# Kernel optimization log

Hardware: AMD Instinct MI355X
Metric: run time of the kernel (lower is better)

The kernel has to match this reference:

```python
import jax, jax.numpy as jnp
import numpy as np

B, S, D, H, HS, FF, L, V = 8, 512, 512, 8, 64, 2048, 6, 1024
EPS = 1e-5


def _layer_norm(x, g, b):
    m = jnp.mean(x, axis=-1, keepdims=True)
    v = jnp.var(x, axis=-1, keepdims=True)
    return (x - m) * jax.lax.rsqrt(v + EPS) * g + b


def _pos_encoding(seq_len, d, dtype):
    # Faithful to source: exponent uses 2*i/seq_len (x.shape[seq_dim]), not d_model.
    pos = jnp.arange(seq_len, dtype=dtype)[:, None]
    i = jnp.arange(d)
    pe = pos / (10000.0 ** (2.0 * i.astype(dtype) / seq_len))
    return jnp.where(i % 2 == 0, jnp.sin(pe), jnp.cos(pe))


def setup_inputs() -> dict:
    key = jax.random.key(0)
    ks = jax.random.split(key, 16)
    tok_ids = jax.random.randint(ks[0], (B, S), 0, V)
    tokens = jax.nn.one_hot(tok_ids, V, dtype=jnp.float32)
    std = 0.02
    return {
        "tokens": tokens,
        "token_embeddings": jax.random.normal(ks[1], (V, D), jnp.float32),
        "qkv_w": jax.random.normal(ks[2], (L, H, D, 3 * HS), jnp.float32) * std,
        "qkv_b": jnp.zeros((L, H, 3 * HS), jnp.float32),
        "out_w": jax.random.normal(ks[3], (L, D, D), jnp.float32) * std,
        "out_b": jnp.zeros((L, D), jnp.float32),
        "w1": jax.random.normal(ks[4], (L, D, FF), jnp.float32) * std,
        "b1": jnp.zeros((L, FF), jnp.float32),
        "w2": jax.random.normal(ks[5], (L, FF, D), jnp.float32) * std,
        "b2": jnp.zeros((L, D), jnp.float32),
        "ln1_g": jnp.ones((L, D), jnp.float32),
        "ln1_b": jnp.zeros((L, D), jnp.float32),
        "ln2_g": jnp.ones((L, D), jnp.float32),
        "ln2_b": jnp.zeros((L, D), jnp.float32),
    }


def _forward(tokens, token_embeddings, qkv_w, qkv_b, out_w, out_b,
             w1, b1, w2, b2, ln1_g, ln1_b, ln2_g, ln2_b):
    dt = tokens.dtype
    x = tokens @ (token_embeddings * (D ** 0.5))          # [B,S,D]
    x = x + _pos_encoding(S, D, dt)
    # Multiplicative causal mask (faithful to source: -1e6 strictly above diag, 0 elsewhere)
    mask = jnp.triu(jnp.full((S, S), -1e6, dt), k=1)
    scale = 1.0 / (HS ** 0.5)

    def block(x, p):
        (qw, qb, ow, ob, w1_, b1_, w2_, b2_, g1, be1, g2, be2) = p
        qkv = jnp.einsum('bsd,hdk->bhsk', x, qw) + qb[None, :, None, :]
        q, k, v = jnp.split(qkv, 3, axis=-1)              # each [B,H,S,HS]
        logits = jnp.einsum('bhsk,bhtk->bhst', q, k)      # [B,H,S,S]
        attn = jax.nn.softmax(logits * mask * scale, axis=-1)
        o = jnp.einsum('bhst,bhtk->bhsk', attn, v)
        o = o.transpose(0, 2, 1, 3).reshape(x.shape[0], S, D)  # concat heads
        o = o @ ow + ob
        x = _layer_norm(x + o, g1, be1)
        h = jax.nn.relu(x @ w1_ + b1_) @ w2_ + b2_
        x = _layer_norm(x + h, g2, be2)
        return x, None

    params = (qkv_w, qkv_b, out_w, out_b, w1, b1, w2, b2, ln1_g, ln1_b, ln2_g, ln2_b)
    x, _ = jax.lax.scan(block, x, params)
    return x @ token_embeddings.T                          # [B,S,V]


def reference(tokens, token_embeddings, qkv_w, qkv_b, out_w, out_b,
              w1, b1, w2, b2, ln1_g, ln1_b, ln2_g, ln2_b):
    return _forward(tokens, token_embeddings, qkv_w, qkv_b, out_w, out_b,
                    w1, b1, w2, b2, ln1_g, ln1_b, ln2_g, ln2_b)
```

## Files before the change

### kernel.cpp

```cpp
#include <hip/hip_runtime.h>
#include <math.h>

#define BB 8
#define SS 512
#define DD 512
#define HH 8
#define HSD 64
#define FFD 2048
#define LL 6
#define VV 1024
#define NROWS (BB*SS)
#define EPS 1e-5f

__global__ __launch_bounds__(256)
void embed_kernel(const float* __restrict__ tokens,
                  const float* __restrict__ emb,
                  float* __restrict__ x)
{
    const int n = blockIdx.x;
    const int s = n & (SS - 1);
    const int t = threadIdx.x;
    __shared__ int sidx;
    #pragma unroll
    for (int r = 0; r < 4; ++r) {
        int v = t + 256 * r;
        if (tokens[(long)n * VV + v] > 0.5f) sidx = v;
    }
    __syncthreads();
    const int idx = sidx;
    const float sq = 22.62741699796952f;
    #pragma unroll
    for (int r = 0; r < 2; ++r) {
        int d = t + 256 * r;
        float e = emb[(long)idx * DD + d] * sq;
        float expo  = (2.0f * (float)d) / 512.0f;
        float denom = powf(10000.0f, expo);
        float val   = (float)s / denom;
        float pe = ((d & 1) == 0) ? sinf(val) : cosf(val);
        x[(long)n * DD + d] = e + pe;
    }
}

__device__ __forceinline__ void gll16(const float* g, float* l)
{
    __builtin_amdgcn_global_load_lds(
        (const __attribute__((address_space(1))) void*)g,
        (__attribute__((address_space(3))) void*)l, 16, 0, 0);
}

template<int TNB, bool BT, bool QKVB, bool BIAS, bool RELU, bool RES>
__global__ __launch_bounds__(256)
void gemm_t(const float* __restrict__ A, const float* __restrict__ B,
            const float* __restrict__ bias, const float* __restrict__ res,
            float* __restrict__ C,
            int M, int N, int K, int lda, int ldb, int ldc)
{
    constexpr int NW   = TNB / 16;
    constexpr int BSTR = BT ? (TNB + 4) : TNB;
    constexpr int CPW  = TNB / 32;
    constexpr int CLOG = (TNB == 128) ? 7 : 6;
    const int t  = threadIdx.x;
    const int w  = t >> 6;
    const int ln = t & 63;
    const int bm = blockIdx.y * 128;
    const int bn = blockIdx.x * TNB;
    __shared__ float As[32][132];
    __shared__ __align__(16) float Bs[32][BSTR];
    const int tx = t & 15;
    const int ty = t >> 4;
    float acc[8][NW] = {};

    for (int k0 = 0; k0 < K; k0 += 32) {
        if (QKVB || !BT) {
            #pragma unroll
            for (int p = 0; p < CPW; ++p) {
                int ch = w * CPW + p;
                int fo = ch * 256 + ln * 4;
                int r  = fo >> CLOG;
                int c  = fo & (TNB - 1);
                const float* src;
                if (QKVB) {
                    int col = bn + c;
                    int hh = (int)((unsigned)col / 192u);
                    int j  = col - hh * 192;
                    src = B + (long)hh * (DD * 192) + (long)(k0 + r) * 192 + j;
                } else {
                    src = B + (long)(k0 + r) * ldb + bn + c;
                }
                gll16(src, &Bs[0][0] + ch * 256);
            }
        } else {
            #pragma unroll
            for (int p = 0; p < TNB / 32; ++p) {
                int q = t + 256 * p;
                int r = q >> 3, kc = (q & 7) * 4;
                float4 b4 = *(const float4*)(B + (long)(bn + r) * ldb + k0 + kc);
                Bs[kc + 0][r] = b4.x; Bs[kc + 1][r] = b4.y;
                Bs[kc + 2][r] = b4.z; Bs[kc + 3][r] = b4.w;
            }
        }
        #pragma unroll
        for (int p = 0; p < 4; ++p) {
            int q = t + 256 * p;
            int r = q >> 3, kc = (q & 7) * 4;
            float4 a4 = *(const float4*)(A + (long)(bm + r) * lda + k0 + kc);
            As[kc + 0][r] = a4.x; As[kc + 1][r] = a4.y;
            As[kc + 2][r] = a4.z; As[kc + 3][r] = a4.w;
        }
        __syncthreads();
        #pragma unroll
        for (int kk = 0; kk < 32; ++kk) {
            float a[8], bv[NW];
            *(float4*)&a[0] = *(const float4*)&As[kk][ty * 8];
            *(float4*)&a[4] = *(const float4*)&As[kk][ty * 8 + 4];
            #pragma unroll
            for (int g = 0; g < NW / 4; ++g)
                *(float4*)&bv[g * 4] = *(const float4*)&Bs[kk][tx * NW + g * 4];
            #pragma unroll
            for (int ii = 0; ii < 8; ++ii)
                #pragma unroll
                for (int jj = 0; jj < NW; ++jj)
                    acc[ii][jj] += a[ii] * bv[jj];
        }
        __syncthreads();
    }

    #pragma unroll
    for (int ii = 0; ii < 8; ++ii) {
        int r = bm + ty * 8 + ii;
        #pragma unroll
        for (int jj = 0; jj < NW; ++jj) {
            int c = bn + tx * NW + jj;
            float v = acc[ii][jj];
            if (BIAS) v += bias[c];
            if (RELU) v = fmaxf(v, 0.0f);
            if (RES)  v += res[(long)r * ldc + c];
            C[(long)r * ldc + c] = v;
        }
    }
}

__global__ __launch_bounds__(256)
void attn_kernel(const float* __restrict__ qkv, float* __restrict__ oc)
{
    const int i0 = blockIdx.x * 16;
    const int h  = blockIdx.y, b = blockIdx.z;
    const int t  = threadIdx.x;
    const int w  = t >> 6;
    const int ln = t & 63;

    __shared__ __align__(16) float Qs[16][64];
    __shared__ __align__(16) float KV[2][64 * 64];
    __shared__ __align__(16) float Zb[16][512];

    const float* __restrict__ base = qkv + (long)b * SS * 1536 + (long)h * 192;

    const int rB = ln >> 4;
    const int g0 = ln & 15;
    const int gx = g0 ^ rB;

    gll16(base + (long)(i0 + 4 * w + rB) * 1536 + g0 * 4, &Qs[4 * w][0]);
    #pragma unroll
    for (int p = 0; p < 4; ++p) {
        int q = 4 * w + p;
        int r = 4 * q + rB;
        int g = (gx ^ (p << 2)) << 2;
        gll16(base + (long)r * 1536 + 64 + g, &KV[0][q * 256]);
    }
    __syncthreads();

    for (int kt = 0; kt < 8; ++kt) {
        const int cur = kt & 1;
        float* nb = &KV[cur ^ 1][0];
        if (kt < 7) {
            const int j0n = (kt + 1) * 64;
            #pragma unroll
            for (int p = 0; p < 4; ++p) {
                int q = 4 * w + p;
                int r = 4 * q + rB;
                int g = (gx ^ (p << 2)) << 2;
                gll16(base + (long)(j0n + r) * 1536 + 64 + g, nb + q * 256);
            }
        } else {
            #pragma unroll
            for (int p = 0; p < 4; ++p) {
                int q = 4 * w + p;
                int r = 4 * q + rB;
                gll16(base + (long)r * 1536 + 128 + g0 * 4, nb + q * 256);
            }
        }

        const float* cb = &KV[cur][0];
        float4 kreg[16];
        #pragma unroll
        for (int kk = 0; kk < 16; ++kk)
            kreg[kk] = *(const float4*)(cb + ln * 64 + ((kk ^ g0) << 2));

        const int j0 = kt * 64;
        #pragma unroll
        for (int c = 0; c < 4; ++c) {
            const int i = 4 * w + c;
            const float4* q4 = (const float4*)&Qs[i][0];
            float dot = 0.0f;
            #pragma unroll
            for (int kk = 0; kk < 16; ++kk) {
                float4 kv = kreg[kk];
                float4 qq = q4[kk];
                dot += qq.x * kv.x + qq.y * kv.y + qq.z * kv.z + qq.w * kv.w;
            }
            const int gi = i0 + i, gj = j0 + ln;
            Zb[i][j0 + ln] = (gj <= gi) ? 0.0f : (dot * -1.0e6f) * 0.125f;
        }
        __syncthreads();
    }

    #pragma unroll
    for (int c = 0; c < 4; ++c) {
        const int i = 4 * w + c;
        float p[8];
        float mx = -3.4e38f;
        #pragma unroll
        for (int r = 0; r < 8; ++r) { p[r] = Zb[i][r * 64 + ln]; mx = fmaxf(mx, p[r]); }
        #pragma unroll
        for (int o = 32; o >= 1; o >>= 1) mx = fmaxf(mx, __shfl_xor(mx, o));
        float sum = 0.0f;
        #pragma unroll
        for (int r = 0; r < 8; ++r) { p[r] = expf(p[r] - mx); sum += p[r]; }
        #pragma unroll
        for (int o = 32; o >= 1; o >>= 1) sum += __shfl_xor(sum, o);
        const float inv = 1.0f / sum;
        #pragma unroll
        for (int r = 0; r < 8; ++r) Zb[i][r * 64 + ln] = p[r] * inv;
    }

    float oA[4] = {0.0f, 0.0f, 0.0f, 0.0f};
    for (int kt = 0; kt < 8; ++kt) {
        const int cur = kt & 1;
        if (kt < 7) {
            float* nb = &KV[cur ^ 1][0];
            const int j0n = (kt + 1) * 64;
            #pragma unroll
            for (int p = 0; p < 4; ++p) {
                int q = 4 * w + p;
                int r = 4 * q + rB;
                gll16(base + (long)(j0n + r) * 1536 + 128 + g0 * 4, nb + q * 256);
            }
        }

        const float* cb = &KV[cur][0];
        float vreg[64];
        #pragma unroll
        for (int kk = 0; kk < 64; ++kk) vreg[kk] = cb[kk * 64 + ln];

        const int j0 = kt * 64;
        #pragma unroll
        for (int c = 0; c < 4; ++c) {
            const int i = 4 * w + c;
            const float4* pr = (const float4*)&Zb[i][j0];
            float acc = oA[c];
            #pragma unroll
            for (int kk = 0; kk < 16; ++kk) {
                float4 pv = pr[kk];
                acc += pv.x * vreg[kk * 4 + 0];
                acc += pv.y * vreg[kk * 4 + 1];
                acc += pv.z * vreg[kk * 4 + 2];
                acc += pv.w * vreg[kk * 4 + 3];
            }
            oA[c] = acc;
        }
        if (kt < 7) __syncthreads();
    }

    #pragma unroll
    for (int c = 0; c < 4; ++c) {
        const int gi = i0 + 4 * w + c;
        oc[(long)(b * SS + gi) * DD + h * HSD + ln] = oA[c];
    }
}

__device__ __forceinline__ float blk_sum(float v, float* sb)
{
    #pragma unroll
    for (int m = 32; m >= 1; m >>= 1) v += __shfl_xor(v, m);
    if ((threadIdx.x & 63) == 0) sb[threadIdx.x >> 6] = v;
    __syncthreads();
    v = sb[0] + sb[1] + sb[2] + sb[3];
    __syncthreads();
    return v;
}

__global__ __launch_bounds__(256)
void ln_kernel(const float* __restrict__ in, const float* __restrict__ g,
               const float* __restrict__ bb, float* __restrict__ out)
{
    __shared__ float sb[4];
    const int n = blockIdx.x;
    const int t = threadIdx.x;
    const float* x = in + (long)n * DD;
    float v0 = x[t], v1 = x[t + 256];
    float total = blk_sum(v0 + v1, sb);
    float mean = total * (1.0f / 512.0f);
    float d0 = v0 - mean, d1 = v1 - mean;
    float ss = blk_sum(d0 * d0 + d1 * d1, sb);
    float var = ss * (1.0f / 512.0f);
    float inv = 1.0f / sqrtf(var + EPS);
    out[(long)n * DD + t]       = d0 * inv * g[t]       + bb[t];
    out[(long)n * DD + t + 256] = d1 * inv * g[t + 256] + bb[t + 256];
}

extern "C" void kernel_launch(void* const* d_in, const int* in_sizes, int n_in,
                              void* d_out, int out_size, void* d_ws, size_t ws_size,
                              hipStream_t stream)
{
    const float* tokens = (const float*)d_in[0];
    const float* emb    = (const float*)d_in[1];
    const float* qkv_w  = (const float*)d_in[2];
    const float* qkv_b  = (const float*)d_in[3];
    const float* out_w  = (const float*)d_in[4];
    const float* out_b  = (const float*)d_in[5];
    const float* w1     = (const float*)d_in[6];
    const float* b1     = (const float*)d_in[7];
    const float* w2     = (const float*)d_in[8];
    const float* b2     = (const float*)d_in[9];
    const float* ln1_g  = (const float*)d_in[10];
    const float* ln1_b  = (const float*)d_in[11];
    const float* ln2_g  = (const float*)d_in[12];
    const float* ln2_b  = (const float*)d_in[13];
    float* out = (float*)d_out;

    float* ws  = (float*)d_ws;
    float* x   = ws;
    float* y   = x  + (long)NROWS * DD;
    float* oc  = y  + (long)NROWS * DD;
    float* big = oc + (long)NROWS * DD;

    embed_kernel<<<NROWS, 256, 0, stream>>>(tokens, emb, x);

    for (int l = 0; l < LL; ++l) {
        const float* qw  = qkv_w + (long)l * HH * DD * 192;
        const float* qb  = qkv_b + (long)l * HH * 192;
        const float* ow  = out_w + (long)l * DD * DD;
        const float* ob  = out_b + (long)l * DD;
        const float* w1l = w1 + (long)l * DD * FFD;
        const float* b1l = b1 + (long)l * FFD;
        const float* w2l = w2 + (long)l * FFD * DD;
        const float* b2l = b2 + (long)l * DD;

        gemm_t<64, false, true, true, false, false><<<dim3(24, 32), 256, 0, stream>>>(
            x, qw, qb, nullptr, big, NROWS, 1536, DD, DD, 192, 1536);

        attn_kernel<<<dim3(SS / 16, HH, BB), 256, 0, stream>>>(big, oc);

        gemm_t<64, false, false, true, false, true><<<dim3(8, 32), 256, 0, stream>>>(
            oc, ow, ob, x, y, NROWS, DD, DD, DD, DD, DD);

        ln_kernel<<<NROWS, 256, 0, stream>>>(y, ln1_g + (long)l * DD, ln1_b + (long)l * DD, x);

        gemm_t<128, false, false, true, true, false><<<dim3(16, 32), 256, 0, stream>>>(
            x, w1l, b1l, nullptr, big, NROWS, FFD, DD, DD, FFD, FFD);

        gemm_t<64, false, false, true, false, true><<<dim3(8, 32), 256, 0, stream>>>(
            big, w2l, b2l, x, y, NROWS, DD, FFD, FFD, DD, DD);

        ln_kernel<<<NROWS, 256, 0, stream>>>(y, ln2_g + (long)l * DD, ln2_b + (long)l * DD, x);
    }

    gemm_t<64, true, false, false, false, false><<<dim3(16, 32), 256, 0, stream>>>(
        x, emb, nullptr, nullptr, out, NROWS, VV, DD, DD, DD, VV);
}
```

Before: 3.826 ms.

## Split-K the D-output GEMMs and fuse partial reduction, bias, residual into layernorm

```diff
diff --git a/kernel.cpp b/kernel.cpp
--- a/kernel.cpp
+++ b/kernel.cpp
@@ -48,7 +48,7 @@
         (__attribute__((address_space(3))) void*)l, 16, 0, 0);
 }
 
-template<int TNB, bool BT, bool QKVB, bool BIAS, bool RELU, bool RES>
+template<int TNB, bool BT, bool QKVB, bool BIAS, bool RELU, bool RES, int SPLITK>
 __global__ __launch_bounds__(256)
 void gemm_t(const float* __restrict__ A, const float* __restrict__ B,
             const float* __restrict__ bias, const float* __restrict__ res,
@@ -70,7 +70,10 @@
     const int ty = t >> 4;
     float acc[8][NW] = {};
 
-    for (int k0 = 0; k0 < K; k0 += 32) {
+    const int kspan = K / SPLITK;
+    const int kbase = (SPLITK > 1) ? blockIdx.z * kspan : 0;
+
+    for (int k0 = kbase; k0 < kbase + kspan; k0 += 32) {
         if (QKVB || !BT) {
             #pragma unroll
             for (int p = 0; p < CPW; ++p) {
@@ -125,6 +128,7 @@
         __syncthreads();
     }
 
+    float* Cp = (SPLITK > 1) ? (C + (long)blockIdx.z * ((long)M * ldc)) : C;
     #pragma unroll
     for (int ii = 0; ii < 8; ++ii) {
         int r = bm + ty * 8 + ii;
@@ -135,7 +139,7 @@
             if (BIAS) v += bias[c];
             if (RELU) v = fmaxf(v, 0.0f);
             if (RES)  v += res[(long)r * ldc + c];
-            C[(long)r * ldc + c] = v;
+            Cp[(long)r * ldc + c] = v;
         }
     }
 }
@@ -289,15 +293,27 @@
     return v;
 }
 
+template<int NP>
 __global__ __launch_bounds__(256)
-void ln_kernel(const float* __restrict__ in, const float* __restrict__ g,
-               const float* __restrict__ bb, float* __restrict__ out)
+void ln_fuse_kernel(const float* __restrict__ P, const float* __restrict__ bias,
+                    const float* __restrict__ res,
+                    const float* __restrict__ g, const float* __restrict__ bb,
+                    float* __restrict__ out)
 {
     __shared__ float sb[4];
     const int n = blockIdx.x;
     const int t = threadIdx.x;
-    const float* x = in + (long)n * DD;
-    float v0 = x[t], v1 = x[t + 256];
+    float v0 = P[(long)n * DD + t];
+    float v1 = P[(long)n * DD + t + 256];
+    #pragma unroll
+    for (int p = 1; p < NP; ++p) {
+        v0 += P[(long)p * NROWS * DD + (long)n * DD + t];
+        v1 += P[(long)p * NROWS * DD + (long)n * DD + t + 256];
+    }
+    v0 += bias[t];       v1 += bias[t + 256];
+    v0 += res[(long)n * DD + t];
+    v1 += res[(long)n * DD + t + 256];
+
     float total = blk_sum(v0 + v1, sb);
     float mean = total * (1.0f / 512.0f);
     float d0 = v0 - mean, d1 = v1 - mean;
@@ -333,6 +349,8 @@
     float* y   = x  + (long)NROWS * DD;
     float* oc  = y  + (long)NROWS * DD;
     float* big = oc + (long)NROWS * DD;
+    float* opP  = big;
+    float* ffP  = y;
 
     embed_kernel<<<NROWS, 256, 0, stream>>>(tokens, emb, x);
 
@@ -346,25 +364,27 @@
         const float* w2l = w2 + (long)l * FFD * DD;
         const float* b2l = b2 + (long)l * DD;
 
-        gemm_t<64, false, true, true, false, false><<<dim3(24, 32), 256, 0, stream>>>(
+        gemm_t<64, false, true, true, false, false, 1><<<dim3(24, 32), 256, 0, stream>>>(
             x, qw, qb, nullptr, big, NROWS, 1536, DD, DD, 192, 1536);
 
         attn_kernel<<<dim3(SS / 16, HH, BB), 256, 0, stream>>>(big, oc);
 
-        gemm_t<64, false, false, true, false, true><<<dim3(8, 32), 256, 0, stream>>>(
-            oc, ow, ob, x, y, NROWS, DD, DD, DD, DD, DD);
-
-        ln_kernel<<<NROWS, 256, 0, stream>>>(y, ln1_g + (long)l * DD, ln1_b + (long)l * DD, x);
-
-        gemm_t<128, false, false, true, true, false><<<dim3(16, 32), 256, 0, stream>>>(
+        gemm_t<64, false, false, false, false, false, 2><<<dim3(8, 32, 2), 256, 0, stream>>>(
+            oc, ow, nullptr, nullptr, opP, NROWS, DD, DD, DD, DD, DD);
+
+        ln_fuse_kernel<2><<<NROWS, 256, 0, stream>>>(
+            opP, ob, x, ln1_g + (long)l * DD, ln1_b + (long)l * DD, x);
+
+        gemm_t<128, false, false, true, true, false, 1><<<dim3(16, 32), 256, 0, stream>>>(
             x, w1l, b1l, nullptr, big, NROWS, FFD, DD, DD, FFD, FFD);
 
-        gemm_t<64, false, false, true, false, true><<<dim3(8, 32), 256, 0, stream>>>(
-            big, w2l, b2l, x, y, NROWS, DD, FFD, FFD, DD, DD);
-
-        ln_kernel<<<NROWS, 256, 0, stream>>>(y, ln2_g + (long)l * DD, ln2_b + (long)l * DD, x);
-    }
-
-    gemm_t<64, true, false, false, false, false><<<dim3(16, 32), 256, 0, stream>>>(
+        gemm_t<64, false, false, false, false, false, 2><<<dim3(8, 32, 2), 256, 0, stream>>>(
+            big, w2l, nullptr, nullptr, ffP, NROWS, DD, FFD, FFD, DD, DD);
+
+        ln_fuse_kernel<2><<<NROWS, 256, 0, stream>>>(
+            ffP, b2l, x, ln2_g + (long)l * DD, ln2_b + (long)l * DD, x);
+    }
+
+    gemm_t<64, true, false, false, false, false, 1><<<dim3(16, 32), 256, 0, stream>>>(
         x, emb, nullptr, nullptr, out, NROWS, VV, DD, DD, DD, VV);
 }
```

After: 3.477 ms. 1.1x faster.

## Split-K the N=512 GEMMs and fuse partial reduction into layernorm

Applied to the files above, without the earlier changes.

```diff
diff --git a/kernel.cpp b/kernel.cpp
--- a/kernel.cpp
+++ b/kernel.cpp
@@ -48,29 +48,36 @@
         (__attribute__((address_space(3))) void*)l, 16, 0, 0);
 }
 
-template<int TNB, bool BT, bool QKVB, bool BIAS, bool RELU, bool RES>
+template<int TNB, int BK, bool BT, bool QKVB, bool BIAS, bool RELU, bool RES, int SPLITK>
 __global__ __launch_bounds__(256)
 void gemm_t(const float* __restrict__ A, const float* __restrict__ B,
             const float* __restrict__ bias, const float* __restrict__ res,
-            float* __restrict__ C,
+            float* __restrict__ C, float* __restrict__ C2,
             int M, int N, int K, int lda, int ldb, int ldc)
 {
     constexpr int NW   = TNB / 16;
-    constexpr int BSTR = BT ? (TNB + 4) : TNB;
-    constexpr int CPW  = TNB / 32;
+    constexpr int KSH  = BK / 4;
+    constexpr int ASH  = (BK == 64) ? 4 : 3;
     constexpr int CLOG = (TNB == 128) ? 7 : 6;
+    constexpr int NCH  = BK * TNB / 256;
+    constexpr int CPW  = NCH / 4;
+    constexpr int AF4  = BK / 8;
+    constexpr int BF4  = TNB * KSH / 256;
     const int t  = threadIdx.x;
     const int w  = t >> 6;
     const int ln = t & 63;
     const int bm = blockIdx.y * 128;
     const int bn = blockIdx.x * TNB;
-    __shared__ float As[32][132];
-    __shared__ __align__(16) float Bs[32][BSTR];
+    __shared__ float As[BK][132];
+    __shared__ __align__(16) float Bs[BK][BT ? (TNB + 4) : TNB];
     const int tx = t & 15;
     const int ty = t >> 4;
     float acc[8][NW] = {};
 
-    for (int k0 = 0; k0 < K; k0 += 32) {
+    const int kspan = K / SPLITK;
+    const int kbase = (SPLITK > 1) ? blockIdx.z * kspan : 0;
+
+    for (int k0 = kbase; k0 < kbase + kspan; k0 += BK) {
         if (QKVB || !BT) {
             #pragma unroll
             for (int p = 0; p < CPW; ++p) {
@@ -91,25 +98,25 @@
             }
         } else {
             #pragma unroll
-            for (int p = 0; p < TNB / 32; ++p) {
+            for (int p = 0; p < BF4; ++p) {
                 int q = t + 256 * p;
-                int r = q >> 3, kc = (q & 7) * 4;
+                int r = q >> ASH, kc = (q & (KSH - 1)) * 4;
                 float4 b4 = *(const float4*)(B + (long)(bn + r) * ldb + k0 + kc);
                 Bs[kc + 0][r] = b4.x; Bs[kc + 1][r] = b4.y;
                 Bs[kc + 2][r] = b4.z; Bs[kc + 3][r] = b4.w;
             }
         }
         #pragma unroll
-        for (int p = 0; p < 4; ++p) {
+        for (int p = 0; p < AF4; ++p) {
             int q = t + 256 * p;
-            int r = q >> 3, kc = (q & 7) * 4;
+            int r = q >> ASH, kc = (q & (KSH - 1)) * 4;
             float4 a4 = *(const float4*)(A + (long)(bm + r) * lda + k0 + kc);
             As[kc + 0][r] = a4.x; As[kc + 1][r] = a4.y;
             As[kc + 2][r] = a4.z; As[kc + 3][r] = a4.w;
         }
         __syncthreads();
         #pragma unroll
-        for (int kk = 0; kk < 32; ++kk) {
+        for (int kk = 0; kk < BK; ++kk) {
             float a[8], bv[NW];
             *(float4*)&a[0] = *(const float4*)&As[kk][ty * 8];
             *(float4*)&a[4] = *(const float4*)&As[kk][ty * 8 + 4];
@@ -125,6 +132,14 @@
         __syncthreads();
     }
 
+    float* Cp;
+    if (SPLITK > 1) {
+        const long mn = (long)M * ldc;
+        const int z = blockIdx.z;
+        Cp = (z < 2) ? (C + (long)z * mn) : (C2 + (long)(z - 2) * mn);
+    } else {
+        Cp = C;
+    }
     #pragma unroll
     for (int ii = 0; ii < 8; ++ii) {
         int r = bm + ty * 8 + ii;
@@ -135,7 +150,7 @@
             if (BIAS) v += bias[c];
             if (RELU) v = fmaxf(v, 0.0f);
             if (RES)  v += res[(long)r * ldc + c];
-            C[(long)r * ldc + c] = v;
+            Cp[(long)r * ldc + c] = v;
         }
     }
 }
@@ -290,22 +305,30 @@
 }
 
 __global__ __launch_bounds__(256)
-void ln_kernel(const float* __restrict__ in, const float* __restrict__ g,
-               const float* __restrict__ bb, float* __restrict__ out)
+void ln_fuse4_kernel(const float* __restrict__ P, const float* __restrict__ P2,
+                     const float* __restrict__ bias, const float* __restrict__ res,
+                     const float* __restrict__ g, const float* __restrict__ bb,
+                     float* __restrict__ out)
 {
     __shared__ float sb[4];
     const int n = blockIdx.x;
     const int t = threadIdx.x;
-    const float* x = in + (long)n * DD;
-    float v0 = x[t], v1 = x[t + 256];
+    const long st = (long)NROWS * DD;
+    const long o0 = (long)n * DD + t;
+    const long o1 = o0 + 256;
+    float v0 = P[o0] + P[st + o0] + P2[o0] + P2[st + o0];
+    float v1 = P[o1] + P[st + o1] + P2[o1] + P2[st + o1];
+    v0 += bias[t];       v1 += bias[t + 256];
+    v0 += res[o0];       v1 += res[o1];
+
     float total = blk_sum(v0 + v1, sb);
     float mean = total * (1.0f / 512.0f);
     float d0 = v0 - mean, d1 = v1 - mean;
     float ss = blk_sum(d0 * d0 + d1 * d1, sb);
     float var = ss * (1.0f / 512.0f);
     float inv = 1.0f / sqrtf(var + EPS);
-    out[(long)n * DD + t]       = d0 * inv * g[t]       + bb[t];
-    out[(long)n * DD + t + 256] = d1 * inv * g[t + 256] + bb[t + 256];
+    out[o0] = d0 * inv * g[t]       + bb[t];
+    out[o1] = d1 * inv * g[t + 256] + bb[t + 256];
 }
 
 extern "C" void kernel_launch(void* const* d_in, const int* in_sizes, int n_in,
@@ -333,6 +356,7 @@
     float* y   = x  + (long)NROWS * DD;
     float* oc  = y  + (long)NROWS * DD;
     float* big = oc + (long)NROWS * DD;
+    const long st = (long)NROWS * DD;
 
     embed_kernel<<<NROWS, 256, 0, stream>>>(tokens, emb, x);
 
@@ -346,25 +370,27 @@
         const float* w2l = w2 + (long)l * FFD * DD;
         const float* b2l = b2 + (long)l * DD;
 
-        gemm_t<64, false, true, true, false, false><<<dim3(24, 32), 256, 0, stream>>>(
-            x, qw, qb, nullptr, big, NROWS, 1536, DD, DD, 192, 1536);
+        gemm_t<64, 64, false, true, true, false, false, 1><<<dim3(24, 32), 256, 0, stream>>>(
+            x, qw, qb, nullptr, big, nullptr, NROWS, 1536, DD, DD, 192, 1536);
 
         attn_kernel<<<dim3(SS / 16, HH, BB), 256, 0, stream>>>(big, oc);
 
-        gemm_t<64, false, false, true, false, true><<<dim3(8, 32), 256, 0, stream>>>(
-            oc, ow, ob, x, y, NROWS, DD, DD, DD, DD, DD);
-
-        ln_kernel<<<NROWS, 256, 0, stream>>>(y, ln1_g + (long)l * DD, ln1_b + (long)l * DD, x);
-
-        gemm_t<128, false, false, true, true, false><<<dim3(16, 32), 256, 0, stream>>>(
-            x, w1l, b1l, nullptr, big, NROWS, FFD, DD, DD, FFD, FFD);
-
-        gemm_t<64, false, false, true, false, true><<<dim3(8, 32), 256, 0, stream>>>(
-            big, w2l, b2l, x, y, NROWS, DD, FFD, FFD, DD, DD);
-
-        ln_kernel<<<NROWS, 256, 0, stream>>>(y, ln2_g + (long)l * DD, ln2_b + (long)l * DD, x);
-    }
-
-    gemm_t<64, true, false, false, false, false><<<dim3(16, 32), 256, 0, stream>>>(
-        x, emb, nullptr, nullptr, out, NROWS, VV, DD, DD, DD, VV);
-}
+        gemm_t<64, 32, false, false, false, false, false, 4><<<dim3(8, 32, 4), 256, 0, stream>>>(
+            oc, ow, nullptr, nullptr, big, big + 2 * st, NROWS, DD, DD, DD, DD, DD);
+
+        ln_fuse4_kernel<<<NROWS, 256, 0, stream>>>(
+            big, big + 2 * st, ob, x, ln1_g + (long)l * DD, ln1_b + (long)l * DD, x);
+
+        gemm_t<128, 64, false, false, true, true, false, 1><<<dim3(16, 32), 256, 0, stream>>>(
+            x, w1l, b1l, nullptr, big, nullptr, NROWS, FFD, DD, DD, FFD, FFD);
+
+        gemm_t<64, 32, false, false, false, false, false, 4><<<dim3(8, 32, 4), 256, 0, stream>>>(
+            big, w2l, nullptr, nullptr, y, out, NROWS, DD, FFD, FFD, DD, DD);
+
+        ln_fuse4_kernel<<<NROWS, 256, 0, stream>>>(
+            y, out, b2l, x, ln2_g + (long)l * DD, ln2_b + (long)l * DD, x);
+    }
+
+    gemm_t<64, 64, true, false, false, false, false, 1><<<dim3(16, 32), 256, 0, stream>>>(
+        x, emb, nullptr, nullptr, out, nullptr, NROWS, VV, DD, DD, DD, VV);
+}
```

New measurement: 3.675 ms. 1.04x faster.
